# Performance work log

Hardware: AMD Instinct MI355X
Metric: run time of the kernel (lower is better)

## Reference

```python
import jax, jax.numpy as jnp
import numpy as np

NUM_HEAD = 2
KR = 3          # kernel_range = [3, 3]
SHIFT = 1
N_P = KR * KR   # 9 taps
PAD = (KR // 2) * SHIFT  # 1
OFFSETS = [(i, j) for i in (-(KR // 2), 0, KR // 2) if True for j in ()]  # placeholder, real list below
OFFSETS = [(i, j) for i in range(-(KR // 2), KR // 2 + 1) for j in range(-(KR // 2), KR // 2 + 1)]


def _conv3x3(x, w, b):
    # x: [B,H,W,Cin], w: [3,3,Cin,Cout] -> SAME conv + bias
    y = jax.lax.conv_general_dilated(
        x, w, window_strides=(1, 1), padding='SAME',
        dimension_numbers=('NHWC', 'HWIO', 'NHWC'))
    return y + b


def setup_inputs() -> dict:
    key = jax.random.key(0)
    B, H, W, D = 4, 128, 128, 64
    ks = jax.random.split(key, 10)
    sc = 0.05  # small init like glorot
    return {
        'x': jax.random.normal(ks[0], (B, H, W, D), jnp.float32),
        # 1x1 conv kernels stored as matrices (equiv. to (1,1,Cin,Cout))
        'K_P': jax.random.normal(ks[1], (D, D * N_P), jnp.float32) * sc,
        'V_P': jax.random.normal(ks[2], (D, D * N_P), jnp.float32) * sc,
        'Q_P': jax.random.normal(ks[3], (D, D), jnp.float32) * sc,
        'ff1_kernel': jax.random.normal(ks[4], (D, D), jnp.float32) * sc,
        'ff1_bias': jax.random.normal(ks[5], (D,), jnp.float32) * sc,
        'ff2_kernel': jax.random.normal(ks[6], (3, 3, D, 2 * D), jnp.float32) * sc,
        'ff2_bias': jax.random.normal(ks[7], (2 * D,), jnp.float32) * sc,
        'ff3_kernel': jax.random.normal(ks[8], (3, 3, 2 * D, D), jnp.float32) * sc,
        'ff3_bias': jax.random.normal(ks[9], (D,), jnp.float32) * sc,
    }


def reference(x, K_P, V_P, Q_P, ff1_kernel, ff1_bias, ff2_kernel, ff2_bias,
              ff3_kernel, ff3_bias):
    B, H, W, D = x.shape
    hd = D // NUM_HEAD

    # 1x1 projections; K/V produce N_P channel chunks, one per tap
    x_k = jnp.einsum('bhwd,de->bhwe', x, K_P).reshape(B, H, W, N_P, D)
    x_v = jnp.einsum('bhwd,de->bhwe', x, V_P).reshape(B, H, W, N_P, D)
    x_q = jnp.einsum('bhwd,de->bhwe', x, Q_P)

    pad5 = ((0, 0), (PAD, PAD), (PAD, PAD), (0, 0), (0, 0))
    k_pad = jnp.pad(x_k, pad5)
    v_pad = jnp.pad(x_v, pad5)

    # tap t uses channel chunk t at spatial offset OFFSETS[t]*SHIFT
    def taps(padded):
        return jnp.stack(
            [padded[:, PAD + i * SHIFT:PAD + i * SHIFT + H,
                    PAD + j * SHIFT:PAD + j * SHIFT + W, t, :]
             for t, (i, j) in enumerate(OFFSETS)], axis=3)  # [B,H,W,N_P,D]

    k_taps = taps(k_pad)
    v_taps = taps(v_pad)

    # validity mask (padded taps get score 0 before softmax, as in original)
    m_pad = jnp.pad(jnp.ones((B, H, W), x.dtype), ((0, 0), (PAD, PAD), (PAD, PAD)))
    mask = jnp.stack(
        [m_pad[:, PAD + i * SHIFT:PAD + i * SHIFT + H,
               PAD + j * SHIFT:PAD + j * SHIFT + W]
         for (i, j) in OFFSETS], axis=3)  # [B,H,W,N_P]

    kh = k_taps.reshape(B, H, W, N_P, NUM_HEAD, hd)
    vh = v_taps.reshape(B, H, W, N_P, NUM_HEAD, hd)
    qh = x_q.reshape(B, H, W, NUM_HEAD, hd)

    # scores per head over taps; masked-multiply then /3, as in original
    scores = jnp.einsum('bhwtnc,bhwnc->bhwnt', kh, qh)
    scores = scores * mask[:, :, :, None, :] / 3.0
    alpha = jax.nn.softmax(scores, axis=-1)  # over taps
    attn = jnp.einsum('bhwnt,bhwtnc->bhwnc', alpha, vh).reshape(B, H, W, D)

    # FFN: 1x1 conv -> relu -> 3x3 conv -> relu -> 3x3 conv -> relu
    t = jax.nn.relu(jnp.einsum('bhwd,de->bhwe', attn, ff1_kernel) + ff1_bias)
    t = jax.nn.relu(_conv3x3(t, ff2_kernel, ff2_bias))
    t = jax.nn.relu(_conv3x3(t, ff3_kernel, ff3_bias))
    return t
```

## Files before the change

kernel.cpp:

```cpp
#include <hip/hip_runtime.h>


typedef _Float16 half8 __attribute__((ext_vector_type(8)));
typedef float f32x4 __attribute__((ext_vector_type(4)));

#define PLANE 524288

__device__ __forceinline__ f32x4 mfma16(half8 a, half8 b, f32x4 c) {
  return __builtin_amdgcn_mfma_f32_16x16x32_f16(a, b, c, 0, 0, 0);
}
__device__ __forceinline__ half8 ldfrag(const _Float16* p) { return *(const half8*)p; }
__device__ __forceinline__ half8 zfrag() { half8 z = {}; return z; }

__device__ __forceinline__ int xcd_swz(int n, int chunk) {
  return (n & 7) * chunk + (n >> 3);
}

__device__ __forceinline__ void gload_lds16(const _Float16* g, _Float16* l) {
  __builtin_amdgcn_global_load_lds(
      (const __attribute__((address_space(1))) void*)g,
      (__attribute__((address_space(3))) void*)l, 16, 0, 0);
}

__global__ __launch_bounds__(256) void prep(
    const float* __restrict__ x, const float* __restrict__ Kp,
    const float* __restrict__ Vp, const float* __restrict__ Qp,
    const float* __restrict__ W1, const float* __restrict__ F2,
    const float* __restrict__ F3, _Float16* __restrict__ xh,
    _Float16* __restrict__ out) {
  if (blockIdx.x < 2048) {
    const int b = xcd_swz(blockIdx.x, 256);
    const int t = threadIdx.x;
    const int px = b * 32 + (t >> 3);
    const int oct = t & 7;
    const float4* s = (const float4*)(x + (size_t)px * 64 + oct * 8);
    float4 a = s[0], b4 = s[1];
    half8 h = { (_Float16)a.x, (_Float16)a.y, (_Float16)a.z, (_Float16)a.w,
                (_Float16)b4.x, (_Float16)b4.y, (_Float16)b4.z, (_Float16)b4.w };
    *(half8*)(xh + (size_t)oct * PLANE + (size_t)px * 8) = h;
    return;
  }
  int e = (blockIdx.x - 2048) * 256 + threadIdx.x;
  int j = e & 7, l = (e >> 3) & 63, f = e >> 9;
  int l15 = l & 15, q8 = (l >> 4) * 8;
  float v;
  if (f < 8)        { int mb = f >> 1, kb = f & 1;
                      v = Qp[(kb*32 + q8 + j) * 64 + mb*16 + l15]; }
  else if (f < 80)  { int g = f - 8, t = g >> 3, mb = (g >> 1) & 3, kb = g & 1;
                      v = Kp[(kb*32 + q8 + j) * 576 + t*64 + mb*16 + l15]; }
  else if (f < 152) { int g = f - 80, t = g >> 3, kb = (g >> 2) & 1, nb = g & 3;
                      v = Vp[(kb*32 + q8 + j) * 576 + t*64 + nb*16 + l15]; }
  else if (f < 160) { int g = f - 152, kb = g >> 2, nb = g & 3;
                      v = W1[(kb*32 + q8 + j) * 64 + nb*16 + l15]; }
  else if (f < 304) { int g = f - 160, t = g >> 4, kb = (g >> 3) & 1, nb = g & 7;
                      v = F2[(t*64 + kb*32 + q8 + j) * 128 + nb*16 + l15]; }
  else              { int g = f - 304, t = g >> 4, kb = (g >> 2) & 3, nb = g & 3;
                      v = F3[(t*128 + kb*32 + q8 + j) * 64 + nb*16 + l15]; }
  out[e] = (_Float16)v;
}

__global__ __launch_bounds__(1024, 4) void attn_ff1(
    const _Float16* __restrict__ xh, const _Float16* __restrict__ wf,
    const float* __restrict__ f1b, _Float16* __restrict__ t1g) {
  extern __shared__ _Float16 smem[];
  const int lane = threadIdx.x & 63, wid = threadIdx.x >> 6;
  const int l15 = lane & 15, q8 = (lane >> 4) * 8;
  const int bid = xcd_swz(blockIdx.x, 32);
  const int row = bid * 2 + (wid >> 3);
  const int rw = wid & 7;
  const int p0 = row * 128 + rw * 16;
  const int h = row & 127;
  const int w0 = rw * 16;
  const int oct0 = lane >> 4;
  float* dent = (float*)(smem + 77824) + wid * 32;

  {
    for (int i = 0; i < 10; ++i) {
      int f = wid * 10 + i;
      if (f < 152)
        gload_lds16(wf + 4096 + (size_t)f * 512 + lane * 8,
                    smem + (size_t)f * 512);
    }
  }

  half8 ax0, ax1;
  {
    const size_t px = (size_t)(p0 + l15);
    ax0 = ldfrag(xh + (size_t)oct0 * PLANE + px * 8);
    ax1 = ldfrag(xh + (size_t)(oct0 + 4) * PLANE + px * 8);
  }
  f32x4 qT[4];
#pragma unroll
  for (int cb = 0; cb < 4; ++cb) {
    half8 aq0 = ldfrag(wf + (cb * 2 + 0) * 512 + lane * 8);
    half8 aq1 = ldfrag(wf + (cb * 2 + 1) * 512 + lane * 8);
    f32x4 c = {};
    c = mfma16(aq0, ax0, c);
    c = mfma16(aq1, ax1, c);
    qT[cb] = c;
  }

  auto load_tap = [&](int t, half8& x0, half8& x1) {
    const int dh = t / 3 - 1, dw = t % 3 - 1;
    const bool rk = (unsigned)(h + dh) < 128u;
    const bool cv = rk && ((unsigned)(w0 + l15 + dw) < 128u);
    const size_t px = (size_t)(p0 + l15 + dh * 128 + dw);
    x0 = cv ? ldfrag(xh + (size_t)oct0 * PLANE + px * 8) : zfrag();
    x1 = cv ? ldfrag(xh + (size_t)(oct0 + 4) * PLANE + px * 8) : zfrag();
  };

  float den0 = 0.f, den1 = 0.f;
  auto score_tap = [&](int t, half8& x0, half8& x1, float& e0, float& e1) {
    const int dh = t / 3 - 1;
    const bool rowok = (unsigned)(h + dh) < 128u;
    half8 kf[8];
    if (rowok) {
#pragma unroll
      for (int f = 0; f < 8; ++f)
        kf[f] = ldfrag(smem + (t * 8 + f) * 512 + lane * 8);
    }
    float pa = 0.f, pb = 0.f;
    if (rowok) {
#pragma unroll
      for (int cb = 0; cb < 4; ++cb) {
        f32x4 c = {};
        c = mfma16(kf[cb * 2 + 0], x0, c);
        c = mfma16(kf[cb * 2 + 1], x1, c);
        float d = qT[cb].x * c.x + qT[cb].y * c.y
                + qT[cb].z * c.z + qT[cb].w * c.w;
        if (cb < 2) pa += d; else pb += d;
      }
      pa += __shfl_xor(pa, 16, 64); pa += __shfl_xor(pa, 32, 64);
      pb += __shfl_xor(pb, 16, 64); pb += __shfl_xor(pb, 32, 64);
    }
    e0 = __expf(pa * (1.f / 3.f));
    e1 = __expf(pb * (1.f / 3.f));
    den0 += e0; den1 += e1;
  };

  half8 q0[3], q1[3];
  load_tap(0, q0[0], q1[0]);
  load_tap(1, q0[1], q1[1]);

  __syncthreads();

  float e0c, e1c;
  score_tap(0, q0[0], q1[0], e0c, e1c);

  const _Float16* BVl = smem + 36864;
  f32x4 at[4];
#pragma unroll
  for (int nb = 0; nb < 4; ++nb) at[nb] = f32x4{};

#pragma unroll
  for (int t = 0; t < 9; ++t) {
    if (t + 2 < 9) load_tap(t + 2, q0[(t + 2) % 3], q1[(t + 2) % 3]);
    const bool rowok = (unsigned)(h + (t / 3 - 1)) < 128u;
    if (rowok) {
      half8 vf[8];
#pragma unroll
      for (int f = 0; f < 8; ++f)
        vf[f] = ldfrag(BVl + (t * 8 + f) * 512 + lane * 8);
      _Float16 h0 = (_Float16)e0c, h1 = (_Float16)e1c;
      half8 b0 = {h0, h0, h0, h0, h0, h0, h0, h0};
      half8 b1 = {h1, h1, h1, h1, h1, h1, h1, h1};
      half8 s00 = q0[t % 3] * b0, s01 = q1[t % 3] * b0;
      half8 s10 = q0[t % 3] * b1, s11 = q1[t % 3] * b1;
#pragma unroll
      for (int nb = 0; nb < 2; ++nb) {
        at[nb]     = mfma16(s00, vf[0 * 4 + nb],     at[nb]);
        at[nb]     = mfma16(s01, vf[1 * 4 + nb],     at[nb]);
        at[nb + 2] = mfma16(s10, vf[0 * 4 + nb + 2], at[nb + 2]);
        at[nb + 2] = mfma16(s11, vf[1 * 4 + nb + 2], at[nb + 2]);
      }
    }
    if (t < 8) {
      float e0n, e1n;
      score_tap(t + 1, q0[(t + 1) % 3], q1[(t + 1) % 3], e0n, e1n);
      e0c = e0n; e1c = e1n;
    }
  }

  dent[0 * 16 + l15] = den0;
  dent[1 * 16 + l15] = den1;
  f32x4 iv[2];
#pragma unroll
  for (int hd = 0; hd < 2; ++hd) {
    f32x4 dv = *(const f32x4*)(dent + hd * 16 + (lane >> 4) * 4);
    iv[hd] = f32x4{1.f / dv.x, 1.f / dv.y, 1.f / dv.z, 1.f / dv.w};
  }

  __syncthreads();
  _Float16* myt = smem + wid * 1152;
#pragma unroll
  for (int nb = 0; nb < 4; ++nb) {
    const int hd = nb >> 1;
#pragma unroll
    for (int r = 0; r < 4; ++r)
      myt[((lane >> 4) * 4 + r) * 72 + nb * 16 + l15] =
          (_Float16)(at[nb][r] * iv[hd][r]);
  }
  const _Float16* B1l = smem + 73728;
  const int pxl = lane >> 2;
  const int co0 = lane & 3;
  half8 aa0 = ldfrag(myt + l15 * 72 + q8);
  half8 aa1 = ldfrag(myt + l15 * 72 + 32 + q8);
#pragma unroll
  for (int nb = 0; nb < 4; ++nb) {
    f32x4 c = {};
    c = mfma16(aa0, ldfrag(B1l + (0 * 4 + nb) * 512 + lane * 8), c);
    c = mfma16(aa1, ldfrag(B1l + (1 * 4 + nb) * 512 + lane * 8), c);
    float bv = f1b[nb * 16 + l15];
#pragma unroll
    for (int r = 0; r < 4; ++r)
      myt[((lane >> 4) * 4 + r) * 72 + nb * 16 + l15] =
          (_Float16)fmaxf(c[r] + bv, 0.f);
  }
  const size_t pxg = (size_t)(p0 + pxl);
  half8 h0 = ldfrag(myt + pxl * 72 + co0 * 8);
  half8 h1 = ldfrag(myt + pxl * 72 + (co0 + 4) * 8);
  *(half8*)(t1g + (size_t)co0 * PLANE + pxg * 8) = h0;
  *(half8*)(t1g + (size_t)(co0 + 4) * PLANE + pxg * 8) = h1;
}

template <int KB, int NBL, int COUT, int DEPTH>
__global__ __launch_bounds__(512, 4) void conv3x3(
    const _Float16* __restrict__ in, const _Float16* __restrict__ wfrag,
    const float* __restrict__ bias, void* __restrict__ outp, int out_fp32) {
  extern __shared__ _Float16 smem[];
  constexpr int NS = DEPTH + 1;
  const int lane = threadIdx.x & 63, wid = threadIdx.x >> 6;
  const int l15 = lane & 15;
  const int bid = xcd_swz(blockIdx.x, 64);
  const int nh = bid & 1;
  const int pairIdx = bid >> 1;
  const int row = pairIdx * 2 + (wid >> 2);
  const int rw = wid & 3;
  const int p0 = row * 128 + rw * 32;
  const int h = row & 127;
  const int w0 = rw * 32;
  const int NBF = COUT / 16;
  const int oct0 = lane >> 4;

  {
    for (int s = 0; s < 9; ++s) {
      int f = wid * 9 + s;
      int t = f >> 3, r = f & 7, kb = r / NBL, i = r % NBL;
      const _Float16* g = wfrag + (size_t)((t * KB + kb) * NBF + nh * NBL + i) * 512;
      gload_lds16(g + lane * 8, smem + f * 512);
    }
  }

  f32x4 acc[2][NBL];
#pragma unroll
  for (int m = 0; m < 2; ++m)
#pragma unroll
    for (int nb = 0; nb < NBL; ++nb) acc[m][nb] = f32x4{};

  auto load_conv = [&](int t, half8 (&dst)[2][KB]) {
    const int dh = t / 3 - 1, dw = t % 3 - 1;
    const bool rk = (unsigned)(h + dh) < 128u;
#pragma unroll
    for (int m = 0; m < 2; ++m) {
      const bool cv = rk && ((unsigned)(w0 + m * 16 + l15 + dw) < 128u);
      const size_t px = (size_t)(p0 + m * 16 + l15 + dh * 128 + dw);
#pragma unroll
      for (int kb = 0; kb < KB; ++kb)
        dst[m][kb] = cv ? ldfrag(in + (size_t)(kb * 4 + oct0) * PLANE + px * 8) : zfrag();
    }
  };

  half8 aq[NS][2][KB];
#pragma unroll
  for (int d = 0; d < DEPTH; ++d) load_conv(d, aq[d]);

  __syncthreads();

#pragma unroll
  for (int t = 0; t < 9; ++t) {
    if (t + DEPTH < 9) load_conv(t + DEPTH, aq[(t + DEPTH) % NS]);
    const bool rowok = (unsigned)(h + (t / 3 - 1)) < 128u;
    if (rowok) {
#pragma unroll
      for (int nb = 0; nb < NBL; ++nb) {
#pragma unroll
        for (int kb = 0; kb < KB; ++kb) {
          half8 b = ldfrag(smem + (size_t)((t * KB + kb) * NBL + nb) * 512 + lane * 8);
          acc[0][nb] = mfma16(aq[t % NS][0][kb], b, acc[0][nb]);
          acc[1][nb] = mfma16(aq[t % NS][1][kb], b, acc[1][nb]);
        }
      }
    }
  }

  if (out_fp32) {
#pragma unroll
    for (int m = 0; m < 2; ++m)
#pragma unroll
      for (int nb = 0; nb < NBL; ++nb) {
        const int ch = nh * NBL * 16 + nb * 16 + l15;
        float bv = bias[ch];
#pragma unroll
        for (int r = 0; r < 4; ++r) {
          float v = fmaxf(acc[m][nb][r] + bv, 0.f);
          size_t px = (size_t)(p0 + m * 16 + (lane >> 4) * 4 + r);
          ((float*)outp)[px * COUT + ch] = v;
        }
      }
  } else {
    __syncthreads();
    _Float16* T = smem + wid * 1152;
    const int pxl = lane >> 2, co0 = lane & 3;
#pragma unroll
    for (int m = 0; m < 2; ++m) {
#pragma unroll
      for (int nb = 0; nb < NBL; ++nb) {
        const int chl = nb * 16 + l15;
        float bv = bias[nh * NBL * 16 + chl];
#pragma unroll
        for (int r = 0; r < 4; ++r)
          T[((lane >> 4) * 4 + r) * 72 + chl] =
              (_Float16)fmaxf(acc[m][nb][r] + bv, 0.f);
      }
      const size_t pxg = (size_t)(p0 + m * 16 + pxl);
      half8 h0 = ldfrag(T + pxl * 72 + co0 * 8);
      half8 h1 = ldfrag(T + pxl * 72 + (co0 + 4) * 8);
      *(half8*)((_Float16*)outp + (size_t)(nh * 8 + co0) * PLANE + pxg * 8) = h0;
      *(half8*)((_Float16*)outp + (size_t)(nh * 8 + co0 + 4) * PLANE + pxg * 8) = h1;
    }
  }
}

__global__ __launch_bounds__(512, 4) void conv3b(
    const _Float16* __restrict__ in, const _Float16* __restrict__ wfrag,
    const float* __restrict__ bias, float* __restrict__ outp) {
  extern __shared__ _Float16 smem[];
  const int lane = threadIdx.x & 63, wid = threadIdx.x >> 6;
  const int l15 = lane & 15;
  const int bid = xcd_swz(blockIdx.x, 64);
  const int nh = bid & 1;
  const int pairIdx = bid >> 1;
  const int row = pairIdx * 2 + (wid >> 2);
  const int rw = wid & 3;
  const int p0 = row * 128 + rw * 32;
  const int h = row & 127;
  const int w0 = rw * 32;
  const int oct0 = lane >> 4;
  const int KB = 4, NBL = 2, NBF = 4, COUT = 64;

  {
    for (int s = 0; s < 9; ++s) {
      int f = wid * 9 + s;
      int t = f >> 3, r = f & 7, kb = r / NBL, i = r % NBL;
      const _Float16* g = wfrag + (size_t)((t * KB + kb) * NBF + nh * NBL + i) * 512;
      gload_lds16(g + lane * 8, smem + f * 512);
    }
  }

  f32x4 acc[2][2];
#pragma unroll
  for (int m = 0; m < 2; ++m)
#pragma unroll
    for (int nb = 0; nb < 2; ++nb) acc[m][nb] = f32x4{};

#pragma unroll
  for (int p = 0; p < 2; ++p) {
    auto load_half = [&](int t, half8 (&dst)[2][2]) {
      const int dh = t / 3 - 1, dw = t % 3 - 1;
      const bool rk = (unsigned)(h + dh) < 128u;
#pragma unroll
      for (int m = 0; m < 2; ++m) {
        const bool cv = rk && ((unsigned)(w0 + m * 16 + l15 + dw) < 128u);
        const size_t px = (size_t)(p0 + m * 16 + l15 + dh * 128 + dw);
#pragma unroll
        for (int kbl = 0; kbl < 2; ++kbl)
          dst[m][kbl] = cv
              ? ldfrag(in + (size_t)((2 * p + kbl) * 4 + oct0) * PLANE + px * 8)
              : zfrag();
      }
    };

    half8 aq[3][2][2];
    load_half(0, aq[0]);
    load_half(1, aq[1]);
    if (p == 0) __syncthreads();

#pragma unroll
    for (int t = 0; t < 9; ++t) {
      if (t + 2 < 9) load_half(t + 2, aq[(t + 2) % 3]);
      const bool rowok = (unsigned)(h + (t / 3 - 1)) < 128u;
      if (rowok) {
#pragma unroll
        for (int nb = 0; nb < 2; ++nb) {
#pragma unroll
          for (int kbl = 0; kbl < 2; ++kbl) {
            half8 b = ldfrag(smem +
                (size_t)((t * KB + 2 * p + kbl) * NBL + nb) * 512 + lane * 8);
            acc[0][nb] = mfma16(aq[t % 3][0][kbl], b, acc[0][nb]);
            acc[1][nb] = mfma16(aq[t % 3][1][kbl], b, acc[1][nb]);
          }
        }
      }
    }
  }

#pragma unroll
  for (int m = 0; m < 2; ++m)
#pragma unroll
    for (int nb = 0; nb < 2; ++nb) {
      const int ch = nh * 32 + nb * 16 + l15;
      float bv = bias[ch];
#pragma unroll
      for (int r = 0; r < 4; ++r) {
        float v = fmaxf(acc[m][nb][r] + bv, 0.f);
        size_t px = (size_t)(p0 + m * 16 + (lane >> 4) * 4 + r);
        outp[px * COUT + ch] = v;
      }
    }
}

extern "C" void kernel_launch(void* const* d_in, const int* in_sizes, int n_in,
                              void* d_out, int out_size, void* d_ws, size_t ws_size,
                              hipStream_t stream) {
  (void)in_sizes; (void)n_in; (void)out_size; (void)ws_size;
  const float* x   = (const float*)d_in[0];
  const float* Kp  = (const float*)d_in[1];
  const float* Vp  = (const float*)d_in[2];
  const float* Qp  = (const float*)d_in[3];
  const float* f1w = (const float*)d_in[4];
  const float* f1b = (const float*)d_in[5];
  const float* f2w = (const float*)d_in[6];
  const float* f2b = (const float*)d_in[7];
  const float* f3w = (const float*)d_in[8];
  const float* f3b = (const float*)d_in[9];

  _Float16* xh  = (_Float16*)d_ws;
  _Float16* wf  = xh + 4194304;
  _Float16* t1g = wf + 229376;
  _Float16* t2g = t1g + 4194304;
  float* outp = (float*)d_out;

  (void)hipFuncSetAttribute((const void*)attn_ff1,
      hipFuncAttributeMaxDynamicSharedMemorySize, 157696);
  (void)hipFuncSetAttribute((const void*)conv3x3<2, 4, 128, 3>,
      hipFuncAttributeMaxDynamicSharedMemorySize, 73728);
  (void)hipFuncSetAttribute((const void*)conv3b,
      hipFuncAttributeMaxDynamicSharedMemorySize, 73728);

  prep<<<2944, 256, 0, stream>>>(x, Kp, Vp, Qp, f1w, f2w, f3w, xh, wf);
  attn_ff1<<<256, 1024, 157696, stream>>>(xh, wf, f1b, t1g);
  conv3x3<2, 4, 128, 3><<<512, 512, 73728, stream>>>(t1g, wf + 81920, f2b, t2g, 0);
  conv3b<<<512, 512, 73728, stream>>>(t2g, wf + 155648, f3b, outp);
}
```

Measured before the change: 135.0 us.

## Fuse attention, ff2 and ff3 into one persistent kernel with neighbor flags

Measured after the change: 517.0 us. +282.9%, slower.

```diff
diff --git a/kernel.cpp b/kernel.cpp
--- a/kernel.cpp
+++ b/kernel.cpp
@@ -20,6 +20,11 @@
   __builtin_amdgcn_global_load_lds(
       (const __attribute__((address_space(1))) void*)g,
       (__attribute__((address_space(3))) void*)l, 16, 0, 0);
+}
+
+__device__ __forceinline__ void spin_flag(const int* f) {
+  while (__hip_atomic_load(f, __ATOMIC_ACQUIRE, __HIP_MEMORY_SCOPE_AGENT) == 0)
+    __builtin_amdgcn_s_sleep(2);
 }
 
 __global__ __launch_bounds__(256) void prep(
@@ -27,7 +32,7 @@
     const float* __restrict__ Vp, const float* __restrict__ Qp,
     const float* __restrict__ W1, const float* __restrict__ F2,
     const float* __restrict__ F3, _Float16* __restrict__ xh,
-    _Float16* __restrict__ out) {
+    _Float16* __restrict__ out, int* __restrict__ flags) {
   if (blockIdx.x < 2048) {
     const int b = xcd_swz(blockIdx.x, 256);
     const int t = threadIdx.x;
@@ -41,6 +46,7 @@
     return;
   }
   int e = (blockIdx.x - 2048) * 256 + threadIdx.x;
+  if (e < 512) flags[e] = 0;
   int j = e & 7, l = (e >> 3) & 63, f = e >> 9;
   int l15 = l & 15, q8 = (l >> 4) * 8;
   float v;
@@ -59,364 +65,351 @@
   out[e] = (_Float16)v;
 }
 
-__global__ __launch_bounds__(1024, 4) void attn_ff1(
+__global__ __launch_bounds__(1024, 4) void mega(
     const _Float16* __restrict__ xh, const _Float16* __restrict__ wf,
-    const float* __restrict__ f1b, _Float16* __restrict__ t1g) {
+    const float* __restrict__ f1b, const float* __restrict__ f2b,
+    const float* __restrict__ f3b, _Float16* __restrict__ t1g,
+    _Float16* __restrict__ t2g, float* __restrict__ outp,
+    int* __restrict__ fl1, int* __restrict__ fl2) {
   extern __shared__ _Float16 smem[];
   const int lane = threadIdx.x & 63, wid = threadIdx.x >> 6;
   const int l15 = lane & 15, q8 = (lane >> 4) * 8;
   const int bid = xcd_swz(blockIdx.x, 32);
-  const int row = bid * 2 + (wid >> 3);
-  const int rw = wid & 7;
-  const int p0 = row * 128 + rw * 16;
-  const int h = row & 127;
-  const int w0 = rw * 16;
   const int oct0 = lane >> 4;
-  float* dent = (float*)(smem + 77824) + wid * 32;
 
   {
+    const int row = bid * 2 + (wid >> 3);
+    const int rw = wid & 7;
+    const int p0 = row * 128 + rw * 16;
+    const int h = row & 127;
+    const int w0 = rw * 16;
+    float* dent = (float*)(smem + 77824) + wid * 32;
+
     for (int i = 0; i < 10; ++i) {
       int f = wid * 10 + i;
       if (f < 152)
         gload_lds16(wf + 4096 + (size_t)f * 512 + lane * 8,
                     smem + (size_t)f * 512);
     }
-  }
-
-  half8 ax0, ax1;
+
+    half8 ax0, ax1;
+    {
+      const size_t px = (size_t)(p0 + l15);
+      ax0 = ldfrag(xh + (size_t)oct0 * PLANE + px * 8);
+      ax1 = ldfrag(xh + (size_t)(oct0 + 4) * PLANE + px * 8);
+    }
+    f32x4 qT[4];
+#pragma unroll
+    for (int cb = 0; cb < 4; ++cb) {
+      half8 aq0 = ldfrag(wf + (cb * 2 + 0) * 512 + lane * 8);
+      half8 aq1 = ldfrag(wf + (cb * 2 + 1) * 512 + lane * 8);
+      f32x4 c = {};
+      c = mfma16(aq0, ax0, c);
+      c = mfma16(aq1, ax1, c);
+      qT[cb] = c;
+    }
+
+    auto load_tap = [&](int t, half8& x0, half8& x1) {
+      const int dh = t / 3 - 1, dw = t % 3 - 1;
+      const bool rk = (unsigned)(h + dh) < 128u;
+      const bool cv = rk && ((unsigned)(w0 + l15 + dw) < 128u);
+      const size_t px = (size_t)(p0 + l15 + dh * 128 + dw);
+      x0 = cv ? ldfrag(xh + (size_t)oct0 * PLANE + px * 8) : zfrag();
+      x1 = cv ? ldfrag(xh + (size_t)(oct0 + 4) * PLANE + px * 8) : zfrag();
+    };
+
+    float den0 = 0.f, den1 = 0.f;
+    auto score_tap = [&](int t, half8& x0, half8& x1, float& e0, float& e1) {
+      const int dh = t / 3 - 1;
+      const bool rowok = (unsigned)(h + dh) < 128u;
+      half8 kf[8];
+      if (rowok) {
+#pragma unroll
+        for (int f = 0; f < 8; ++f)
+          kf[f] = ldfrag(smem + (t * 8 + f) * 512 + lane * 8);
+      }
+      float pa = 0.f, pb = 0.f;
+      if (rowok) {
+#pragma unroll
+        for (int cb = 0; cb < 4; ++cb) {
+          f32x4 c = {};
+          c = mfma16(kf[cb * 2 + 0], x0, c);
+          c = mfma16(kf[cb * 2 + 1], x1, c);
+          float d = qT[cb].x * c.x + qT[cb].y * c.y
+                  + qT[cb].z * c.z + qT[cb].w * c.w;
+          if (cb < 2) pa += d; else pb += d;
+        }
+        pa += __shfl_xor(pa, 16, 64); pa += __shfl_xor(pa, 32, 64);
+        pb += __shfl_xor(pb, 16, 64); pb += __shfl_xor(pb, 32, 64);
+      }
+      e0 = __expf(pa * (1.f / 3.f));
+      e1 = __expf(pb * (1.f / 3.f));
+      den0 += e0; den1 += e1;
+    };
+
+    half8 q0[3], q1[3];
+    load_tap(0, q0[0], q1[0]);
+    load_tap(1, q0[1], q1[1]);
+
+    __syncthreads();
+
+    float e0c, e1c;
+    score_tap(0, q0[0], q1[0], e0c, e1c);
+
+    const _Float16* BVl = smem + 36864;
+    f32x4 at[4];
+#pragma unroll
+    for (int nb = 0; nb < 4; ++nb) at[nb] = f32x4{};
+
+#pragma unroll
+    for (int t = 0; t < 9; ++t) {
+      if (t + 2 < 9) load_tap(t + 2, q0[(t + 2) % 3], q1[(t + 2) % 3]);
+      const bool rowok = (unsigned)(h + (t / 3 - 1)) < 128u;
+      if (rowok) {
+        half8 vf[8];
+#pragma unroll
+        for (int f = 0; f < 8; ++f)
+          vf[f] = ldfrag(BVl + (t * 8 + f) * 512 + lane * 8);
+        _Float16 h0 = (_Float16)e0c, h1 = (_Float16)e1c;
+        half8 b0 = {h0, h0, h0, h0, h0, h0, h0, h0};
+        half8 b1 = {h1, h1, h1, h1, h1, h1, h1, h1};
+        half8 s00 = q0[t % 3] * b0, s01 = q1[t % 3] * b0;
+        half8 s10 = q0[t % 3] * b1, s11 = q1[t % 3] * b1;
+#pragma unroll
+        for (int nb = 0; nb < 2; ++nb) {
+          at[nb]     = mfma16(s00, vf[0 * 4 + nb],     at[nb]);
+          at[nb]     = mfma16(s01, vf[1 * 4 + nb],     at[nb]);
+          at[nb + 2] = mfma16(s10, vf[0 * 4 + nb + 2], at[nb + 2]);
+          at[nb + 2] = mfma16(s11, vf[1 * 4 + nb + 2], at[nb + 2]);
+        }
+      }
+      if (t < 8) {
+        float e0n, e1n;
+        score_tap(t + 1, q0[(t + 1) % 3], q1[(t + 1) % 3], e0n, e1n);
+        e0c = e0n; e1c = e1n;
+      }
+    }
+
+    dent[0 * 16 + l15] = den0;
+    dent[1 * 16 + l15] = den1;
+    f32x4 iv[2];
+#pragma unroll
+    for (int hd = 0; hd < 2; ++hd) {
+      f32x4 dv = *(const f32x4*)(dent + hd * 16 + (lane >> 4) * 4);
+      iv[hd] = f32x4{1.f / dv.x, 1.f / dv.y, 1.f / dv.z, 1.f / dv.w};
+    }
+
+    __syncthreads();
+    _Float16* myt = smem + wid * 1152;
+#pragma unroll
+    for (int nb = 0; nb < 4; ++nb) {
+      const int hd = nb >> 1;
+#pragma unroll
+      for (int r = 0; r < 4; ++r)
+        myt[((lane >> 4) * 4 + r) * 72 + nb * 16 + l15] =
+            (_Float16)(at[nb][r] * iv[hd][r]);
+    }
+    const _Float16* B1l = smem + 73728;
+    const int pxl = lane >> 2;
+    const int co0 = lane & 3;
+    half8 aa0 = ldfrag(myt + l15 * 72 + q8);
+    half8 aa1 = ldfrag(myt + l15 * 72 + 32 + q8);
+#pragma unroll
+    for (int nb = 0; nb < 4; ++nb) {
+      f32x4 c = {};
+      c = mfma16(aa0, ldfrag(B1l + (0 * 4 + nb) * 512 + lane * 8), c);
+      c = mfma16(aa1, ldfrag(B1l + (1 * 4 + nb) * 512 + lane * 8), c);
+      float bv = f1b[nb * 16 + l15];
+#pragma unroll
+      for (int r = 0; r < 4; ++r)
+        myt[((lane >> 4) * 4 + r) * 72 + nb * 16 + l15] =
+            (_Float16)fmaxf(c[r] + bv, 0.f);
+    }
+    const size_t pxg = (size_t)(p0 + pxl);
+    half8 h0 = ldfrag(myt + pxl * 72 + co0 * 8);
+    half8 h1 = ldfrag(myt + pxl * 72 + (co0 + 4) * 8);
+    *(half8*)(t1g + (size_t)co0 * PLANE + pxg * 8) = h0;
+    *(half8*)(t1g + (size_t)(co0 + 4) * PLANE + pxg * 8) = h1;
+  }
+
+  __threadfence();
+  __syncthreads();
+  if (threadIdx.x == 0)
+    __hip_atomic_store(fl1 + bid, 1, __ATOMIC_RELEASE, __HIP_MEMORY_SCOPE_AGENT);
   {
-    const size_t px = (size_t)(p0 + l15);
-    ax0 = ldfrag(xh + (size_t)oct0 * PLANE + px * 8);
-    ax1 = ldfrag(xh + (size_t)(oct0 + 4) * PLANE + px * 8);
-  }
-  f32x4 qT[4];
-#pragma unroll
-  for (int cb = 0; cb < 4; ++cb) {
-    half8 aq0 = ldfrag(wf + (cb * 2 + 0) * 512 + lane * 8);
-    half8 aq1 = ldfrag(wf + (cb * 2 + 1) * 512 + lane * 8);
-    f32x4 c = {};
-    c = mfma16(aq0, ax0, c);
-    c = mfma16(aq1, ax1, c);
-    qT[cb] = c;
-  }
-
-  auto load_tap = [&](int t, half8& x0, half8& x1) {
-    const int dh = t / 3 - 1, dw = t % 3 - 1;
-    const bool rk = (unsigned)(h + dh) < 128u;
-    const bool cv = rk && ((unsigned)(w0 + l15 + dw) < 128u);
-    const size_t px = (size_t)(p0 + l15 + dh * 128 + dw);
-    x0 = cv ? ldfrag(xh + (size_t)oct0 * PLANE + px * 8) : zfrag();
-    x1 = cv ? ldfrag(xh + (size_t)(oct0 + 4) * PLANE + px * 8) : zfrag();
-  };
-
-  float den0 = 0.f, den1 = 0.f;
-  auto score_tap = [&](int t, half8& x0, half8& x1, float& e0, float& e1) {
-    const int dh = t / 3 - 1;
-    const bool rowok = (unsigned)(h + dh) < 128u;
-    half8 kf[8];
-    if (rowok) {
-#pragma unroll
-      for (int f = 0; f < 8; ++f)
-        kf[f] = ldfrag(smem + (t * 8 + f) * 512 + lane * 8);
-    }
-    float pa = 0.f, pb = 0.f;
-    if (rowok) {
-#pragma unroll
-      for (int cb = 0; cb < 4; ++cb) {
-        f32x4 c = {};
-        c = mfma16(kf[cb * 2 + 0], x0, c);
-        c = mfma16(kf[cb * 2 + 1], x1, c);
-        float d = qT[cb].x * c.x + qT[cb].y * c.y
-                + qT[cb].z * c.z + qT[cb].w * c.w;
-        if (cb < 2) pa += d; else pb += d;
-      }
-      pa += __shfl_xor(pa, 16, 64); pa += __shfl_xor(pa, 32, 64);
-      pb += __shfl_xor(pb, 16, 64); pb += __shfl_xor(pb, 32, 64);
-    }
-    e0 = __expf(pa * (1.f / 3.f));
-    e1 = __expf(pb * (1.f / 3.f));
-    den0 += e0; den1 += e1;
-  };
-
-  half8 q0[3], q1[3];
-  load_tap(0, q0[0], q1[0]);
-  load_tap(1, q0[1], q1[1]);
-
-  __syncthreads();
-
-  float e0c, e1c;
-  score_tap(0, q0[0], q1[0], e0c, e1c);
-
-  const _Float16* BVl = smem + 36864;
-  f32x4 at[4];
-#pragma unroll
-  for (int nb = 0; nb < 4; ++nb) at[nb] = f32x4{};
-
-#pragma unroll
-  for (int t = 0; t < 9; ++t) {
-    if (t + 2 < 9) load_tap(t + 2, q0[(t + 2) % 3], q1[(t + 2) % 3]);
-    const bool rowok = (unsigned)(h + (t / 3 - 1)) < 128u;
-    if (rowok) {
-      half8 vf[8];
-#pragma unroll
-      for (int f = 0; f < 8; ++f)
-        vf[f] = ldfrag(BVl + (t * 8 + f) * 512 + lane * 8);
-      _Float16 h0 = (_Float16)e0c, h1 = (_Float16)e1c;
-      half8 b0 = {h0, h0, h0, h0, h0, h0, h0, h0};
-      half8 b1 = {h1, h1, h1, h1, h1, h1, h1, h1};
-      half8 s00 = q0[t % 3] * b0, s01 = q1[t % 3] * b0;
-      half8 s10 = q0[t % 3] * b1, s11 = q1[t % 3] * b1;
-#pragma unroll
-      for (int nb = 0; nb < 2; ++nb) {
-        at[nb]     = mfma16(s00, vf[0 * 4 + nb],     at[nb]);
-        at[nb]     = mfma16(s01, vf[1 * 4 + nb],     at[nb]);
-        at[nb + 2] = mfma16(s10, vf[0 * 4 + nb + 2], at[nb + 2]);
-        at[nb + 2] = mfma16(s11, vf[1 * 4 + nb + 2], at[nb + 2]);
-      }
-    }
-    if (t < 8) {
-      float e0n, e1n;
-      score_tap(t + 1, q0[(t + 1) % 3], q1[(t + 1) % 3], e0n, e1n);
-      e0c = e0n; e1c = e1n;
-    }
-  }
-
-  dent[0 * 16 + l15] = den0;
-  dent[1 * 16 + l15] = den1;
-  f32x4 iv[2];
-#pragma unroll
-  for (int hd = 0; hd < 2; ++hd) {
-    f32x4 dv = *(const f32x4*)(dent + hd * 16 + (lane >> 4) * 4);
-    iv[hd] = f32x4{1.f / dv.x, 1.f / dv.y, 1.f / dv.z, 1.f / dv.w};
-  }
-
-  __syncthreads();
-  _Float16* myt = smem + wid * 1152;
-#pragma unroll
-  for (int nb = 0; nb < 4; ++nb) {
-    const int hd = nb >> 1;
-#pragma unroll
-    for (int r = 0; r < 4; ++r)
-      myt[((lane >> 4) * 4 + r) * 72 + nb * 16 + l15] =
-          (_Float16)(at[nb][r] * iv[hd][r]);
-  }
-  const _Float16* B1l = smem + 73728;
-  const int pxl = lane >> 2;
-  const int co0 = lane & 3;
-  half8 aa0 = ldfrag(myt + l15 * 72 + q8);
-  half8 aa1 = ldfrag(myt + l15 * 72 + 32 + q8);
-#pragma unroll
-  for (int nb = 0; nb < 4; ++nb) {
-    f32x4 c = {};
-    c = mfma16(aa0, ldfrag(B1l + (0 * 4 + nb) * 512 + lane * 8), c);
-    c = mfma16(aa1, ldfrag(B1l + (1 * 4 + nb) * 512 + lane * 8), c);
-    float bv = f1b[nb * 16 + l15];
-#pragma unroll
-    for (int r = 0; r < 4; ++r)
-      myt[((lane >> 4) * 4 + r) * 72 + nb * 16 + l15] =
-          (_Float16)fmaxf(c[r] + bv, 0.f);
-  }
-  const size_t pxg = (size_t)(p0 + pxl);
-  half8 h0 = ldfrag(myt + pxl * 72 + co0 * 8);
-  half8 h1 = ldfrag(myt + pxl * 72 + (co0 + 4) * 8);
-  *(half8*)(t1g + (size_t)co0 * PLANE + pxg * 8) = h0;
-  *(half8*)(t1g + (size_t)(co0 + 4) * PLANE + pxg * 8) = h1;
-}
-
-template <int KB, int NBL, int COUT, int DEPTH>
-__global__ __launch_bounds__(512, 4) void conv3x3(
-    const _Float16* __restrict__ in, const _Float16* __restrict__ wfrag,
-    const float* __restrict__ bias, void* __restrict__ outp, int out_fp32) {
-  extern __shared__ _Float16 smem[];
-  constexpr int NS = DEPTH + 1;
-  const int lane = threadIdx.x & 63, wid = threadIdx.x >> 6;
-  const int l15 = lane & 15;
-  const int bid = xcd_swz(blockIdx.x, 64);
-  const int nh = bid & 1;
-  const int pairIdx = bid >> 1;
-  const int row = pairIdx * 2 + (wid >> 2);
-  const int rw = wid & 3;
-  const int p0 = row * 128 + rw * 32;
-  const int h = row & 127;
-  const int w0 = rw * 32;
-  const int NBF = COUT / 16;
-  const int oct0 = lane >> 4;
-
-  {
+    const _Float16* wf2 = wf + 81920;
     for (int s = 0; s < 9; ++s) {
       int f = wid * 9 + s;
-      int t = f >> 3, r = f & 7, kb = r / NBL, i = r % NBL;
-      const _Float16* g = wfrag + (size_t)((t * KB + kb) * NBF + nh * NBL + i) * 512;
-      gload_lds16(g + lane * 8, smem + f * 512);
-    }
-  }
-
-  f32x4 acc[2][NBL];
-#pragma unroll
-  for (int m = 0; m < 2; ++m)
-#pragma unroll
-    for (int nb = 0; nb < NBL; ++nb) acc[m][nb] = f32x4{};
-
-  auto load_conv = [&](int t, half8 (&dst)[2][KB]) {
-    const int dh = t / 3 - 1, dw = t % 3 - 1;
-    const bool rk = (unsigned)(h + dh) < 128u;
+      int nh = f / 72, r = f % 72;
+      int t = r >> 3, q = r & 7, kb = q >> 2, nb = q & 3;
+      gload_lds16(wf2 + (size_t)((t * 2 + kb) * 8 + nh * 4 + nb) * 512 + lane * 8,
+                  smem + (size_t)f * 512);
+    }
+  }
+  if (threadIdx.x == 0 && (bid & 63) != 0) spin_flag(fl1 + bid - 1);
+  if (threadIdx.x == 64 && (bid & 63) != 63) spin_flag(fl1 + bid + 1);
+  __syncthreads();
+  __threadfence();
+
+  {
+    const int nh = wid >> 3, w2 = wid & 7;
+    const int row = bid * 2 + (w2 >> 2);
+    const int rw = w2 & 3;
+    const int p0 = row * 128 + rw * 32;
+    const int h = row & 127;
+    const int w0 = rw * 32;
+
+    f32x4 acc[2][4];
+#pragma unroll
+    for (int m = 0; m < 2; ++m)
+#pragma unroll
+      for (int nb = 0; nb < 4; ++nb) acc[m][nb] = f32x4{};
+
+    auto load2 = [&](int t, half8 (&dst)[2][2]) {
+      const int dh = t / 3 - 1, dw = t % 3 - 1;
+      const bool rk = (unsigned)(h + dh) < 128u;
+#pragma unroll
+      for (int m = 0; m < 2; ++m) {
+        const bool cv = rk && ((unsigned)(w0 + m * 16 + l15 + dw) < 128u);
+        const size_t px = (size_t)(p0 + m * 16 + l15 + dh * 128 + dw);
+#pragma unroll
+        for (int kb = 0; kb < 2; ++kb)
+          dst[m][kb] = cv ? ldfrag(t1g + (size_t)(kb * 4 + oct0) * PLANE + px * 8)
+                          : zfrag();
+      }
+    };
+
+    half8 aq[3][2][2];
+    load2(0, aq[0]);
+    load2(1, aq[1]);
+
+#pragma unroll
+    for (int t = 0; t < 9; ++t) {
+      if (t + 2 < 9) load2(t + 2, aq[(t + 2) % 3]);
+      const bool rowok = (unsigned)(h + (t / 3 - 1)) < 128u;
+      if (rowok) {
+#pragma unroll
+        for (int nb = 0; nb < 4; ++nb) {
+#pragma unroll
+          for (int kb = 0; kb < 2; ++kb) {
+            half8 b = ldfrag(smem +
+                (size_t)(nh * 72 + (t * 2 + kb) * 4 + nb) * 512 + lane * 8);
+            acc[0][nb] = mfma16(aq[t % 3][0][kb], b, acc[0][nb]);
+            acc[1][nb] = mfma16(aq[t % 3][1][kb], b, acc[1][nb]);
+          }
+        }
+      }
+    }
+
+    __syncthreads();
+    _Float16* T = smem + wid * 1152;
+    const int pxl = lane >> 2, co0 = lane & 3;
 #pragma unroll
     for (int m = 0; m < 2; ++m) {
-      const bool cv = rk && ((unsigned)(w0 + m * 16 + l15 + dw) < 128u);
-      const size_t px = (size_t)(p0 + m * 16 + l15 + dh * 128 + dw);
-#pragma unroll
-      for (int kb = 0; kb < KB; ++kb)
-        dst[m][kb] = cv ? ldfrag(in + (size_t)(kb * 4 + oct0) * PLANE + px * 8) : zfrag();
-    }
-  };
-
-  half8 aq[NS][2][KB];
-#pragma unroll
-  for (int d = 0; d < DEPTH; ++d) load_conv(d, aq[d]);
-
+#pragma unroll
+      for (int nb = 0; nb < 4; ++nb) {
+        const int chl = nb * 16 + l15;
+        float bv = f2b[nh * 64 + chl];
+#pragma unroll
+        for (int r = 0; r < 4; ++r)
+          T[((lane >> 4) * 4 + r) * 72 + chl] =
+              (_Float16)fmaxf(acc[m][nb][r] + bv, 0.f);
+      }
+      const size_t pxg = (size_t)(p0 + m * 16 + pxl);
+      half8 h0 = ldfrag(T + pxl * 72 + co0 * 8);
+      half8 h1 = ldfrag(T + pxl * 72 + (co0 + 4) * 8);
+      *(half8*)(t2g + (size_t)(nh * 8 + co0) * PLANE + pxg * 8) = h0;
+      *(half8*)(t2g + (size_t)(nh * 8 + co0 + 4) * PLANE + pxg * 8) = h1;
+    }
+  }
+
+  __threadfence();
   __syncthreads();
-
-#pragma unroll
-  for (int t = 0; t < 9; ++t) {
-    if (t + DEPTH < 9) load_conv(t + DEPTH, aq[(t + DEPTH) % NS]);
-    const bool rowok = (unsigned)(h + (t / 3 - 1)) < 128u;
-    if (rowok) {
-#pragma unroll
-      for (int nb = 0; nb < NBL; ++nb) {
-#pragma unroll
-        for (int kb = 0; kb < KB; ++kb) {
-          half8 b = ldfrag(smem + (size_t)((t * KB + kb) * NBL + nb) * 512 + lane * 8);
-          acc[0][nb] = mfma16(aq[t % NS][0][kb], b, acc[0][nb]);
-          acc[1][nb] = mfma16(aq[t % NS][1][kb], b, acc[1][nb]);
-        }
-      }
-    }
-  }
-
-  if (out_fp32) {
+  if (threadIdx.x == 0)
+    __hip_atomic_store(fl2 + bid, 1, __ATOMIC_RELEASE, __HIP_MEMORY_SCOPE_AGENT);
+  {
+    const _Float16* wf3 = wf + 155648;
+    for (int s = 0; s < 9; ++s) {
+      int f = wid * 9 + s;
+      int nh = f / 72, r = f % 72;
+      int t = r >> 3, q = r & 7, kb = q >> 1, i = q & 1;
+      gload_lds16(wf3 + (size_t)((t * 4 + kb) * 4 + nh * 2 + i) * 512 + lane * 8,
+                  smem + (size_t)f * 512);
+    }
+  }
+  if (threadIdx.x == 0 && (bid & 63) != 0) spin_flag(fl2 + bid - 1);
+  if (threadIdx.x == 64 && (bid & 63) != 63) spin_flag(fl2 + bid + 1);
+  __syncthreads();
+  __threadfence();
+
+  {
+    const int nh = wid >> 3, w3 = wid & 7;
+    const int row = bid * 2 + (w3 >> 2);
+    const int rw = w3 & 3;
+    const int p0 = row * 128 + rw * 32;
+    const int h = row & 127;
+    const int w0 = rw * 32;
+
+    f32x4 acc[2][2];
 #pragma unroll
     for (int m = 0; m < 2; ++m)
 #pragma unroll
-      for (int nb = 0; nb < NBL; ++nb) {
-        const int ch = nh * NBL * 16 + nb * 16 + l15;
-        float bv = bias[ch];
+      for (int nb = 0; nb < 2; ++nb) acc[m][nb] = f32x4{};
+
+#pragma unroll
+    for (int p = 0; p < 2; ++p) {
+      auto load3 = [&](int t, half8 (&dst)[2][2]) {
+        const int dh = t / 3 - 1, dw = t % 3 - 1;
+        const bool rk = (unsigned)(h + dh) < 128u;
+#pragma unroll
+        for (int m = 0; m < 2; ++m) {
+          const bool cv = rk && ((unsigned)(w0 + m * 16 + l15 + dw) < 128u);
+          const size_t px = (size_t)(p0 + m * 16 + l15 + dh * 128 + dw);
+#pragma unroll
+          for (int kbl = 0; kbl < 2; ++kbl)
+            dst[m][kbl] = cv
+                ? ldfrag(t2g + (size_t)((2 * p + kbl) * 4 + oct0) * PLANE + px * 8)
+                : zfrag();
+        }
+      };
+
+      half8 aq[3][2][2];
+      load3(0, aq[0]);
+      load3(1, aq[1]);
+
+#pragma unroll
+      for (int t = 0; t < 9; ++t) {
+        if (t + 2 < 9) load3(t + 2, aq[(t + 2) % 3]);
+        const bool rowok = (unsigned)(h + (t / 3 - 1)) < 128u;
+        if (rowok) {
+#pragma unroll
+          for (int nb = 0; nb < 2; ++nb) {
+#pragma unroll
+            for (int kbl = 0; kbl < 2; ++kbl) {
+              half8 b = ldfrag(smem +
+                  (size_t)(nh * 72 + (t * 4 + 2 * p + kbl) * 2 + nb) * 512 + lane * 8);
+              acc[0][nb] = mfma16(aq[t % 3][0][kbl], b, acc[0][nb]);
+              acc[1][nb] = mfma16(aq[t % 3][1][kbl], b, acc[1][nb]);
+            }
+          }
+        }
+      }
+    }
+
+#pragma unroll
+    for (int m = 0; m < 2; ++m)
+#pragma unroll
+      for (int nb = 0; nb < 2; ++nb) {
+        const int ch = nh * 32 + nb * 16 + l15;
+        float bv = f3b[ch];
 #pragma unroll
         for (int r = 0; r < 4; ++r) {
           float v = fmaxf(acc[m][nb][r] + bv, 0.f);
           size_t px = (size_t)(p0 + m * 16 + (lane >> 4) * 4 + r);
-          ((float*)outp)[px * COUT + ch] = v;
-        }
-      }
-  } else {
-    __syncthreads();
-    _Float16* T = smem + wid * 1152;
-    const int pxl = lane >> 2, co0 = lane & 3;
-#pragma unroll
-    for (int m = 0; m < 2; ++m) {
-#pragma unroll
-      for (int nb = 0; nb < NBL; ++nb) {
-        const int chl = nb * 16 + l15;
-        float bv = bias[nh * NBL * 16 + chl];
-#pragma unroll
-        for (int r = 0; r < 4; ++r)
-          T[((lane >> 4) * 4 + r) * 72 + chl] =
-              (_Float16)fmaxf(acc[m][nb][r] + bv, 0.f);
-      }
-      const size_t pxg = (size_t)(p0 + m * 16 + pxl);
-      half8 h0 = ldfrag(T + pxl * 72 + co0 * 8);
-      half8 h1 = ldfrag(T + pxl * 72 + (co0 + 4) * 8);
-      *(half8*)((_Float16*)outp + (size_t)(nh * 8 + co0) * PLANE + pxg * 8) = h0;
-      *(half8*)((_Float16*)outp + (size_t)(nh * 8 + co0 + 4) * PLANE + pxg * 8) = h1;
-    }
-  }
-}
-
-__global__ __launch_bounds__(512, 4) void conv3b(
-    const _Float16* __restrict__ in, const _Float16* __restrict__ wfrag,
-    const float* __restrict__ bias, float* __restrict__ outp) {
-  extern __shared__ _Float16 smem[];
-  const int lane = threadIdx.x & 63, wid = threadIdx.x >> 6;
-  const int l15 = lane & 15;
-  const int bid = xcd_swz(blockIdx.x, 64);
-  const int nh = bid & 1;
-  const int pairIdx = bid >> 1;
-  const int row = pairIdx * 2 + (wid >> 2);
-  const int rw = wid & 3;
-  const int p0 = row * 128 + rw * 32;
-  const int h = row & 127;
-  const int w0 = rw * 32;
-  const int oct0 = lane >> 4;
-  const int KB = 4, NBL = 2, NBF = 4, COUT = 64;
-
-  {
-    for (int s = 0; s < 9; ++s) {
-      int f = wid * 9 + s;
-      int t = f >> 3, r = f & 7, kb = r / NBL, i = r % NBL;
-      const _Float16* g = wfrag + (size_t)((t * KB + kb) * NBF + nh * NBL + i) * 512;
-      gload_lds16(g + lane * 8, smem + f * 512);
-    }
-  }
-
-  f32x4 acc[2][2];
-#pragma unroll
-  for (int m = 0; m < 2; ++m)
-#pragma unroll
-    for (int nb = 0; nb < 2; ++nb) acc[m][nb] = f32x4{};
-
-#pragma unroll
-  for (int p = 0; p < 2; ++p) {
-    auto load_half = [&](int t, half8 (&dst)[2][2]) {
-      const int dh = t / 3 - 1, dw = t % 3 - 1;
-      const bool rk = (unsigned)(h + dh) < 128u;
-#pragma unroll
-      for (int m = 0; m < 2; ++m) {
-        const bool cv = rk && ((unsigned)(w0 + m * 16 + l15 + dw) < 128u);
-        const size_t px = (size_t)(p0 + m * 16 + l15 + dh * 128 + dw);
-#pragma unroll
-        for (int kbl = 0; kbl < 2; ++kbl)
-          dst[m][kbl] = cv
-              ? ldfrag(in + (size_t)((2 * p + kbl) * 4 + oct0) * PLANE + px * 8)
-              : zfrag();
-      }
-    };
-
-    half8 aq[3][2][2];
-    load_half(0, aq[0]);
-    load_half(1, aq[1]);
-    if (p == 0) __syncthreads();
-
-#pragma unroll
-    for (int t = 0; t < 9; ++t) {
-      if (t + 2 < 9) load_half(t + 2, aq[(t + 2) % 3]);
-      const bool rowok = (unsigned)(h + (t / 3 - 1)) < 128u;
-      if (rowok) {
-#pragma unroll
-        for (int nb = 0; nb < 2; ++nb) {
-#pragma unroll
-          for (int kbl = 0; kbl < 2; ++kbl) {
-            half8 b = ldfrag(smem +
-                (size_t)((t * KB + 2 * p + kbl) * NBL + nb) * 512 + lane * 8);
-            acc[0][nb] = mfma16(aq[t % 3][0][kbl], b, acc[0][nb]);
-            acc[1][nb] = mfma16(aq[t % 3][1][kbl], b, acc[1][nb]);
-          }
-        }
-      }
-    }
-  }
-
-#pragma unroll
-  for (int m = 0; m < 2; ++m)
-#pragma unroll
-    for (int nb = 0; nb < 2; ++nb) {
-      const int ch = nh * 32 + nb * 16 + l15;
-      float bv = bias[ch];
-#pragma unroll
-      for (int r = 0; r < 4; ++r) {
-        float v = fmaxf(acc[m][nb][r] + bv, 0.f);
-        size_t px = (size_t)(p0 + m * 16 + (lane >> 4) * 4 + r);
-        outp[px * COUT + ch] = v;
-      }
-    }
+          outp[px * 64 + ch] = v;
+        }
+      }
+  }
 }
 
 extern "C" void kernel_launch(void* const* d_in, const int* in_sizes, int n_in,
@@ -438,17 +431,15 @@
   _Float16* wf  = xh + 4194304;
   _Float16* t1g = wf + 229376;
   _Float16* t2g = t1g + 4194304;
+  int* flags = (int*)((char*)d_ws + 34013184);
+  int* fl1 = flags;
+  int* fl2 = flags + 256;
   float* outp = (float*)d_out;
 
-  (void)hipFuncSetAttribute((const void*)attn_ff1,
+  (void)hipFuncSetAttribute((const void*)mega,
       hipFuncAttributeMaxDynamicSharedMemorySize, 157696);
-  (void)hipFuncSetAttribute((const void*)conv3x3<2, 4, 128, 3>,
-      hipFuncAttributeMaxDynamicSharedMemorySize, 73728);
-  (void)hipFuncSetAttribute((const void*)conv3b,
-      hipFuncAttributeMaxDynamicSharedMemorySize, 73728);
-
-  prep<<<2944, 256, 0, stream>>>(x, Kp, Vp, Qp, f1w, f2w, f3w, xh, wf);
-  attn_ff1<<<256, 1024, 157696, stream>>>(xh, wf, f1b, t1g);
-  conv3x3<2, 4, 128, 3><<<512, 512, 73728, stream>>>(t1g, wf + 81920, f2b, t2g, 0);
-  conv3b<<<512, 512, 73728, stream>>>(t2g, wf + 155648, f3b, outp);
-}
+
+  prep<<<2944, 256, 0, stream>>>(x, Kp, Vp, Qp, f1w, f2w, f3w, xh, wf, flags);
+  mega<<<256, 1024, 157696, stream>>>(xh, wf, f1b, f2b, f3b, t1g, t2g, outp,
+                                      fl1, fl2);
+}
```
